# Optimization experiments

Measured on AMD Instinct MI355X. Metric: run time of the kernel, lower is better.

## Reference

```python
import jax, jax.numpy as jnp
import numpy as np

N, D_IN, D_OUT, N_CLASSES = 4096, 1024, 256, 64


def setup_inputs() -> dict:
    key = jax.random.key(0)
    k1, k2, k3, k4 = jax.random.split(key, 4)
    x = jax.random.normal(k1, (N, D_IN), dtype=jnp.float32)
    W = jax.random.normal(k2, (D_IN, D_OUT), dtype=jnp.float32) * 0.02
    b = jax.random.normal(k3, (D_OUT,), dtype=jnp.float32) * 0.02
    targets = jax.random.randint(k4, (N,), 0, N_CLASSES, dtype=jnp.int64)
    return {"x": x, "W": W, "b": b, "targets": targets}


def reference(x, W, b, targets):
    # FC projection (activation = 'linear')
    h = jnp.matmul(x, W) + b                      # [N, d]
    # Pairwise euclidean distances D[i, j] = ||h_i - h_j||_2, matching
    # tf.norm(tf.abs(anchor - others), axis=1) in the original per-anchor loop.
    sq = jnp.sum(h * h, axis=1)                   # [N]
    d2 = sq[:, None] + sq[None, :] - 2.0 * jnp.matmul(h, h.T)
    dist = jnp.sqrt(jnp.maximum(d2, 0.0))         # [N, N]
    same = targets[:, None] == targets[None, :]   # class_division mask
    inf = jnp.float32(np.inf)
    # Hardest positive: max distance among same-class (includes self at 0,
    hardest_pos = jnp.max(jnp.where(same, dist, -inf), axis=1)  # [N]
    # Hardest negative: min distance among different-class samples.
    hardest_neg = jnp.min(jnp.where(same, inf, dist), axis=1)   # [N]
    loss = jnp.sum(jnp.log1p(jnp.exp(hardest_pos - hardest_neg)))
    return loss
```

## Files before the change

kernel.cpp:

```cpp
#include <hip/hip_runtime.h>
#include <math.h>

#define NROWS 4096
#define DIN   1024
#define DOUT  256
#define NPAIR 528

using bfrag = __attribute__((ext_vector_type(8))) short;
using ffrag = __attribute__((ext_vector_type(4))) float;


static __device__ __forceinline__ unsigned short f2bf(float f) {
    unsigned int u = __float_as_uint(f);
    u = (u + 0x7fffu + ((u >> 16) & 1u)) >> 16;
    return (unsigned short)u;
}
static __device__ __forceinline__ unsigned int pack2(float lo, float hi) {
    return (unsigned int)f2bf(lo) | ((unsigned int)f2bf(hi) << 16);
}
static __device__ __forceinline__ unsigned int fkey(float f) {
    unsigned int b = __float_as_uint(f);
    return (b & 0x80000000u) ? ~b : (b | 0x80000000u);
}
static __device__ __forceinline__ float funkey(unsigned int u) {
    return __uint_as_float((u & 0x80000000u) ? (u & 0x7fffffffu) : ~u);
}

__global__ __launch_bounds__(256) void setup(const float* __restrict__ W,
                                             unsigned short* __restrict__ Ws,
                                             float* __restrict__ sq,
                                             unsigned int* __restrict__ pmaxk,
                                             unsigned int* __restrict__ pmink,
                                             float* __restrict__ out) {
    const int f = blockIdx.x * 256 + threadIdx.x;
    {
        const int l  = f & 63;
        const int ks = (f >> 6) & 31;
        const int nt = f >> 11;
        const int col = nt * 16 + (l & 15);
        const int k0  = ks * 32 + (l >> 4) * 8;
        float a[8];
#pragma unroll
        for (int j = 0; j < 8; ++j) a[j] = W[(size_t)(k0 + j) * DOUT + col];
        uint4 v;
        v.x = pack2(a[0], a[1]);
        v.y = pack2(a[2], a[3]);
        v.z = pack2(a[4], a[5]);
        v.w = pack2(a[6], a[7]);
        *(uint4*)&Ws[(size_t)f * 8] = v;
    }
    if (f < NROWS) {
        sq[f]    = 0.0f;
        pmaxk[f] = 0u;
        pmink[f] = 0xFFFFFFFFu;
    }
    if (f == 0) *out = 0.0f;
}

__global__ __launch_bounds__(1024) void gemm1_direct(
    const float* __restrict__ x, const unsigned short* __restrict__ Ws,
    const float* __restrict__ b,
    unsigned short* __restrict__ hs, float* __restrict__ sq) {
    __shared__ __align__(16) short Axs[32 * 528];
    __shared__ __align__(16) short T[16][16][36];

    const int tid = threadIdx.x;
    const int w   = tid >> 6;
    const int l   = tid & 63;
    const int m16 = l & 15;
    const int q   = l >> 4;
    const int t   = blockIdx.x;

    const float* xrow = x + (size_t)(t * 16 + w) * DIN;
#pragma unroll
    for (int s = 0; s < 2; ++s) {
        const int c = s * 512 + l * 8;
        const float4 p0 = *(const float4*)(xrow + c);
        const float4 p1 = *(const float4*)(xrow + c + 4);
        uint4 v;
        v.x = pack2(p0.x, p0.y);
        v.y = pack2(p0.z, p0.w);
        v.z = pack2(p1.x, p1.y);
        v.w = pack2(p1.z, p1.w);
        const int ks = c >> 5;
        const int lw = ((c >> 3) & 3) * 16 + w;
        *(uint4*)&Axs[ks * 528 + lw * 8] = v;
    }
    __syncthreads();

    const bfrag* B = (const bfrag*)Ws + ((size_t)w * 32) * 64 + l;
    ffrag acc = {};
#pragma unroll
    for (int ks = 0; ks < 32; ++ks) {
        const bfrag a = *(const bfrag*)&Axs[ks * 528 + l * 8];
        acc = __builtin_amdgcn_mfma_f32_16x16x32_bf16(a, B[ks * 64], acc, 0, 0, 0);
    }

    const float bc = b[w * 16 + m16];
    float hv[4];
#pragma unroll
    for (int reg = 0; reg < 4; ++reg) hv[reg] = acc[reg] + bc;

#pragma unroll
    for (int reg = 0; reg < 4; ++reg) {
        float p = hv[reg] * hv[reg];
#pragma unroll
        for (int mask = 1; mask < 16; mask <<= 1) p += __shfl_xor(p, mask);
        if (m16 == 0) atomicAdd(&sq[t * 16 + q * 4 + reg], p);
    }

#pragma unroll
    for (int reg = 0; reg < 4; ++reg)
        T[w][q * 4 + reg][m16] = f2bf(hv[reg]);
    __syncthreads();

    if (tid < 512) {
        const int ks = tid >> 6;
        const int ll = tid & 63;
        const int qq = ll >> 4;
        bfrag v = *(const bfrag*)&T[2 * ks + (qq >> 1)][ll & 15][(qq & 1) * 8];
        ((bfrag*)hs)[((size_t)t * 8 + ks) * 64 + ll] = v;
    }
}

__global__ __launch_bounds__(256) void hardest_tri(
    const unsigned short* __restrict__ hs, const float* __restrict__ sq,
    const int* __restrict__ targets,
    unsigned int* __restrict__ pmaxk, unsigned int* __restrict__ pmink) {
    const int tid = threadIdx.x;
    const int w   = tid >> 6;
    const int wi  = w & 1, wj = w >> 1;
    const int l   = tid & 63;
    const int m16 = l & 15;
    const int q   = l >> 4;

    const int k = blockIdx.x;
    int bj = (int)((sqrtf(8.0f * (float)k + 1.0f) - 1.0f) * 0.5f);
    while ((bj + 1) * (bj + 2) / 2 <= k) ++bj;
    while (bj * (bj + 1) / 2 > k) --bj;
    const int bi = k - bj * (bj + 1) / 2;
    const bool diag = (bi == bj);

    const int iw = bi * 128 + wi * 64;
    const int jw = bj * 128 + wj * 64;
    const int tA = iw >> 4;
    const int tB = jw >> 4;

    ffrag acc[4][4] = {};

#pragma unroll
    for (int ks = 0; ks < 8; ++ks) {
        bfrag a[4], bb[4];
#pragma unroll
        for (int mi = 0; mi < 4; ++mi)
            a[mi] = *(const bfrag*)&hs[(((size_t)(tA + mi) * 8 + ks) * 64 + l) * 8];
#pragma unroll
        for (int nj = 0; nj < 4; ++nj)
            bb[nj] = *(const bfrag*)&hs[(((size_t)(tB + nj) * 8 + ks) * 64 + l) * 8];
#pragma unroll
        for (int mi = 0; mi < 4; ++mi)
#pragma unroll
            for (int nj = 0; nj < 4; ++nj)
                acc[mi][nj] = __builtin_amdgcn_mfma_f32_16x16x32_bf16(
                    a[mi], bb[nj], acc[mi][nj], 0, 0, 0);
    }

    int   tj[4];
    float svj[4];
#pragma unroll
    for (int nj = 0; nj < 4; ++nj) {
        const int col = jw + nj * 16 + m16;
        tj[nj]  = targets[col];
        svj[nj] = sq[col];
    }

    float cmx[4], cmn[4];
#pragma unroll
    for (int nj = 0; nj < 4; ++nj) { cmx[nj] = -INFINITY; cmn[nj] = INFINITY; }

#pragma unroll
    for (int mi = 0; mi < 4; ++mi)
#pragma unroll
        for (int reg = 0; reg < 4; ++reg) {
            const int row = iw + mi * 16 + q * 4 + reg;
            const int ti  = targets[row];
            const float si = sq[row];
            float mx = -INFINITY, mn = INFINITY;
#pragma unroll
            for (int nj = 0; nj < 4; ++nj) {
                const float g    = acc[mi][nj][reg];
                const float vrow = fmaf(-2.0f, g, svj[nj]);
                const float vcol = fmaf(-2.0f, g, si);
                if (tj[nj] == ti) {
                    mx = fmaxf(mx, vrow);
                    cmx[nj] = fmaxf(cmx[nj], vcol);
                } else {
                    mn = fminf(mn, vrow);
                    cmn[nj] = fminf(cmn[nj], vcol);
                }
            }
#pragma unroll
            for (int mask = 1; mask < 16; mask <<= 1) {
                mx = fmaxf(mx, __shfl_xor(mx, mask));
                mn = fminf(mn, __shfl_xor(mn, mask));
            }
            if (m16 == 0) {
                atomicMax(&pmaxk[row], fkey(mx));
                atomicMin(&pmink[row], fkey(mn));
            }
        }

    if (!diag) {
#pragma unroll
        for (int nj = 0; nj < 4; ++nj) {
            float mx = cmx[nj], mn = cmn[nj];
            mx = fmaxf(mx, __shfl_xor(mx, 16));
            mn = fminf(mn, __shfl_xor(mn, 16));
            mx = fmaxf(mx, __shfl_xor(mx, 32));
            mn = fminf(mn, __shfl_xor(mn, 32));
            if (q == 0) {
                const int col = jw + nj * 16 + m16;
                atomicMax(&pmaxk[col], fkey(mx));
                atomicMin(&pmink[col], fkey(mn));
            }
        }
    }
}

__global__ __launch_bounds__(256) void finalize(const float* __restrict__ sq,
                                                const unsigned int* __restrict__ pmaxk,
                                                const unsigned int* __restrict__ pmink,
                                                float* __restrict__ out) {
    __shared__ float wsum[4];
    const int i = blockIdx.x * 256 + threadIdx.x;
    const float mp = funkey(pmaxk[i]);
    const float mn = funkey(pmink[i]);
    const float si = sq[i];
    const float hp = sqrtf(fmaxf(si + mp, 0.0f));
    const float hn = sqrtf(fmaxf(si + mn, 0.0f));
    const float d  = hp - hn;
    float li = fmaxf(d, 0.0f) + log1pf(expf(-fabsf(d)));
#pragma unroll
    for (int off = 32; off; off >>= 1) li += __shfl_down(li, off);
    const int lane = threadIdx.x & 63, wv = threadIdx.x >> 6;
    if (lane == 0) wsum[wv] = li;
    __syncthreads();
    if (threadIdx.x == 0)
        atomicAdd(out, wsum[0] + wsum[1] + wsum[2] + wsum[3]);
}

extern "C" void kernel_launch(void* const* d_in, const int* in_sizes, int n_in,
                              void* d_out, int out_size, void* d_ws, size_t ws_size,
                              hipStream_t stream) {
    const float* x       = (const float*)d_in[0];
    const float* W       = (const float*)d_in[1];
    const float* b       = (const float*)d_in[2];
    const int*   targets = (const int*)d_in[3];
    float* out = (float*)d_out;

    unsigned short* Ws    = (unsigned short*)d_ws;
    unsigned short* hs    = Ws + DOUT * DIN;
    float*          sq    = (float*)(hs + NROWS * DOUT);
    unsigned int*   pmaxk = (unsigned int*)(sq + NROWS);
    unsigned int*   pmink = pmaxk + NROWS;

    setup<<<16 * 32 * 64 / 256, 256, 0, stream>>>(W, Ws, sq, pmaxk, pmink, out);
    gemm1_direct<<<NROWS / 16, 1024, 0, stream>>>(x, Ws, b, hs, sq);
    hardest_tri<<<NPAIR, 256, 0, stream>>>(hs, sq, targets, pmaxk, pmink);
    finalize<<<NROWS / 256, 256, 0, stream>>>(sq, pmaxk, pmink, out);
}
```

Measured before the change: 98.36 us.

## Fuse all four stages into one persistent kernel with grid barriers

Replaces the setup, GEMM, pairwise-hardest and finalize launches with a single persistent kernel of 512 blocks that uses atomic-counter grid barriers between phases. The projection GEMM is split into half-width blocks of 256 threads, each computing two output tiles per wave. The aim is to remove inter-kernel launch gaps and tail effects. In exchange it adds global barrier spin costs, relies on all 512 blocks being co-resident, and adds a memset launch to reset the barrier counter.

```diff
diff --git a/kernel.cpp b/kernel.cpp
--- a/kernel.cpp
+++ b/kernel.cpp
@@ -5,6 +5,7 @@
 #define DIN   1024
 #define DOUT  256
 #define NPAIR 528
+#define GRID  512
 
 using bfrag = __attribute__((ext_vector_type(8))) short;
 using ffrag = __attribute__((ext_vector_type(4))) float;
@@ -26,19 +27,40 @@
     return __uint_as_float((u & 0x80000000u) ? (u & 0x7fffffffu) : ~u);
 }
 
-__global__ __launch_bounds__(256) void setup(const float* __restrict__ W,
-                                             unsigned short* __restrict__ Ws,
-                                             float* __restrict__ sq,
-                                             unsigned int* __restrict__ pmaxk,
-                                             unsigned int* __restrict__ pmink,
-                                             float* __restrict__ out) {
-    const int f = blockIdx.x * 256 + threadIdx.x;
-    {
-        const int l  = f & 63;
+static __device__ __forceinline__ void gridbar(unsigned int* bar, unsigned int target) {
+    __syncthreads();
+    if (threadIdx.x == 0) {
+        __hip_atomic_fetch_add(bar, 1u, __ATOMIC_ACQ_REL, __HIP_MEMORY_SCOPE_AGENT);
+        while (__hip_atomic_load(bar, __ATOMIC_ACQUIRE, __HIP_MEMORY_SCOPE_AGENT) < target)
+            __builtin_amdgcn_s_sleep(1);
+    }
+    __syncthreads();
+}
+
+__global__ __launch_bounds__(256, 2) void fused(
+    const float* __restrict__ x, const float* __restrict__ W,
+    const float* __restrict__ bv, const int* __restrict__ targets,
+    unsigned short* __restrict__ Ws, unsigned short* __restrict__ hs,
+    float* __restrict__ sq, unsigned int* __restrict__ pmaxk,
+    unsigned int* __restrict__ pmink, unsigned int* __restrict__ bar,
+    float* __restrict__ out) {
+    __shared__ __align__(16) short Axs[32 * 528];
+    __shared__ __align__(16) short T[8][16][36];
+    __shared__ float wsum[4];
+
+    const int tid = threadIdx.x;
+    const int bid = blockIdx.x;
+    const int w   = tid >> 6;
+    const int l   = tid & 63;
+    const int m16 = l & 15;
+    const int q   = l >> 4;
+
+    if (tid < 64) {
+        const int f  = bid * 64 + tid;
         const int ks = (f >> 6) & 31;
         const int nt = f >> 11;
-        const int col = nt * 16 + (l & 15);
-        const int k0  = ks * 32 + (l >> 4) * 8;
+        const int col = nt * 16 + m16;
+        const int k0  = ks * 32 + q * 8;
         float a[8];
 #pragma unroll
         for (int j = 0; j < 8; ++j) a[j] = W[(size_t)(k0 + j) * DOUT + col];
@@ -48,205 +70,196 @@
         v.z = pack2(a[4], a[5]);
         v.w = pack2(a[6], a[7]);
         *(uint4*)&Ws[(size_t)f * 8] = v;
-    }
-    if (f < NROWS) {
-        sq[f]    = 0.0f;
-        pmaxk[f] = 0u;
-        pmink[f] = 0xFFFFFFFFu;
-    }
-    if (f == 0) *out = 0.0f;
-}
-
-__global__ __launch_bounds__(1024) void gemm1_direct(
-    const float* __restrict__ x, const unsigned short* __restrict__ Ws,
-    const float* __restrict__ b,
-    unsigned short* __restrict__ hs, float* __restrict__ sq) {
-    __shared__ __align__(16) short Axs[32 * 528];
-    __shared__ __align__(16) short T[16][16][36];
-
-    const int tid = threadIdx.x;
-    const int w   = tid >> 6;
-    const int l   = tid & 63;
-    const int m16 = l & 15;
-    const int q   = l >> 4;
-    const int t   = blockIdx.x;
-
-    const float* xrow = x + (size_t)(t * 16 + w) * DIN;
-#pragma unroll
-    for (int s = 0; s < 2; ++s) {
-        const int c = s * 512 + l * 8;
-        const float4 p0 = *(const float4*)(xrow + c);
-        const float4 p1 = *(const float4*)(xrow + c + 4);
-        uint4 v;
-        v.x = pack2(p0.x, p0.y);
-        v.y = pack2(p0.z, p0.w);
-        v.z = pack2(p1.x, p1.y);
-        v.w = pack2(p1.z, p1.w);
-        const int ks = c >> 5;
-        const int lw = ((c >> 3) & 3) * 16 + w;
-        *(uint4*)&Axs[ks * 528 + lw * 8] = v;
-    }
-    __syncthreads();
-
-    const bfrag* B = (const bfrag*)Ws + ((size_t)w * 32) * 64 + l;
-    ffrag acc = {};
-#pragma unroll
-    for (int ks = 0; ks < 32; ++ks) {
-        const bfrag a = *(const bfrag*)&Axs[ks * 528 + l * 8];
-        acc = __builtin_amdgcn_mfma_f32_16x16x32_bf16(a, B[ks * 64], acc, 0, 0, 0);
-    }
-
-    const float bc = b[w * 16 + m16];
-    float hv[4];
-#pragma unroll
-    for (int reg = 0; reg < 4; ++reg) hv[reg] = acc[reg] + bc;
-
-#pragma unroll
-    for (int reg = 0; reg < 4; ++reg) {
-        float p = hv[reg] * hv[reg];
-#pragma unroll
-        for (int mask = 1; mask < 16; mask <<= 1) p += __shfl_xor(p, mask);
-        if (m16 == 0) atomicAdd(&sq[t * 16 + q * 4 + reg], p);
-    }
-
-#pragma unroll
-    for (int reg = 0; reg < 4; ++reg)
-        T[w][q * 4 + reg][m16] = f2bf(hv[reg]);
-    __syncthreads();
-
-    if (tid < 512) {
-        const int ks = tid >> 6;
-        const int ll = tid & 63;
-        const int qq = ll >> 4;
-        bfrag v = *(const bfrag*)&T[2 * ks + (qq >> 1)][ll & 15][(qq & 1) * 8];
-        ((bfrag*)hs)[((size_t)t * 8 + ks) * 64 + ll] = v;
-    }
-}
-
-__global__ __launch_bounds__(256) void hardest_tri(
-    const unsigned short* __restrict__ hs, const float* __restrict__ sq,
-    const int* __restrict__ targets,
-    unsigned int* __restrict__ pmaxk, unsigned int* __restrict__ pmink) {
-    const int tid = threadIdx.x;
-    const int w   = tid >> 6;
-    const int wi  = w & 1, wj = w >> 1;
-    const int l   = tid & 63;
-    const int m16 = l & 15;
-    const int q   = l >> 4;
-
-    const int k = blockIdx.x;
-    int bj = (int)((sqrtf(8.0f * (float)k + 1.0f) - 1.0f) * 0.5f);
-    while ((bj + 1) * (bj + 2) / 2 <= k) ++bj;
-    while (bj * (bj + 1) / 2 > k) --bj;
-    const int bi = k - bj * (bj + 1) / 2;
-    const bool diag = (bi == bj);
-
-    const int iw = bi * 128 + wi * 64;
-    const int jw = bj * 128 + wj * 64;
-    const int tA = iw >> 4;
-    const int tB = jw >> 4;
-
-    ffrag acc[4][4] = {};
-
-#pragma unroll
-    for (int ks = 0; ks < 8; ++ks) {
-        bfrag a[4], bb[4];
+    } else if (tid < 72) {
+        const int i = bid * 8 + (tid - 64);
+        sq[i]    = 0.0f;
+        pmaxk[i] = 0u;
+        pmink[i] = 0xFFFFFFFFu;
+    } else if (tid == 72 && bid == 0) {
+        *out = 0.0f;
+    }
+    gridbar(bar, GRID);
+
+    {
+        const int t    = bid >> 1;
+        const int half = bid & 1;
+
+#pragma unroll
+        for (int rr = 0; rr < 4; ++rr) {
+            const int row = w * 4 + rr;
+            const float* xrow = x + (size_t)(t * 16 + row) * DIN;
+#pragma unroll
+            for (int s = 0; s < 2; ++s) {
+                const int c = s * 512 + l * 8;
+                const float4 p0 = *(const float4*)(xrow + c);
+                const float4 p1 = *(const float4*)(xrow + c + 4);
+                uint4 v;
+                v.x = pack2(p0.x, p0.y);
+                v.y = pack2(p0.z, p0.w);
+                v.z = pack2(p1.x, p1.y);
+                v.w = pack2(p1.z, p1.w);
+                const int ks = c >> 5;
+                const int lw = ((c >> 3) & 3) * 16 + row;
+                *(uint4*)&Axs[ks * 528 + lw * 8] = v;
+            }
+        }
+        __syncthreads();
+
+        const int nt0 = half * 8 + w * 2;
+        const bfrag* B0 = (const bfrag*)Ws + ((size_t)nt0 * 32) * 64 + l;
+        ffrag acc0 = {};
+        ffrag acc1 = {};
+#pragma unroll
+        for (int ks = 0; ks < 32; ++ks) {
+            const bfrag a = *(const bfrag*)&Axs[ks * 528 + l * 8];
+            acc0 = __builtin_amdgcn_mfma_f32_16x16x32_bf16(a, B0[ks * 64], acc0, 0, 0, 0);
+            acc1 = __builtin_amdgcn_mfma_f32_16x16x32_bf16(a, B0[2048 + ks * 64], acc1, 0, 0, 0);
+        }
+
+        float pr[4];
+        {
+            const float bc0 = bv[nt0 * 16 + m16];
+            const float bc1 = bv[(nt0 + 1) * 16 + m16];
+#pragma unroll
+            for (int reg = 0; reg < 4; ++reg) {
+                const float h0 = acc0[reg] + bc0;
+                const float h1 = acc1[reg] + bc1;
+                pr[reg] = h0 * h0 + h1 * h1;
+                T[w * 2][q * 4 + reg][m16]     = f2bf(h0);
+                T[w * 2 + 1][q * 4 + reg][m16] = f2bf(h1);
+            }
+        }
+#pragma unroll
+        for (int reg = 0; reg < 4; ++reg) {
+            float pp = pr[reg];
+#pragma unroll
+            for (int mask = 1; mask < 16; mask <<= 1) pp += __shfl_xor(pp, mask);
+            if (m16 == 0) atomicAdd(&sq[t * 16 + q * 4 + reg], pp);
+        }
+        __syncthreads();
+
+        {
+            const int ksl = tid >> 6;
+            const int ks  = half * 4 + ksl;
+            const int qq  = l >> 4;
+            bfrag v = *(const bfrag*)&T[2 * ksl + (qq >> 1)][l & 15][(qq & 1) * 8];
+            ((bfrag*)hs)[((size_t)t * 8 + ks) * 64 + l] = v;
+        }
+    }
+    gridbar(bar, 2 * GRID);
+
+    for (int k = bid; k < NPAIR; k += GRID) {
+        const int wi = w & 1, wj = w >> 1;
+
+        int bj = (int)((sqrtf(8.0f * (float)k + 1.0f) - 1.0f) * 0.5f);
+        while ((bj + 1) * (bj + 2) / 2 <= k) ++bj;
+        while (bj * (bj + 1) / 2 > k) --bj;
+        const int bi = k - bj * (bj + 1) / 2;
+        const bool diag = (bi == bj);
+
+        const int iw = bi * 128 + wi * 64;
+        const int jw = bj * 128 + wj * 64;
+        const int tA = iw >> 4;
+        const int tB = jw >> 4;
+
+        ffrag acc[4][4] = {};
+
+#pragma unroll
+        for (int ks = 0; ks < 8; ++ks) {
+            bfrag a[4], bb[4];
+#pragma unroll
+            for (int mi = 0; mi < 4; ++mi)
+                a[mi] = *(const bfrag*)&hs[(((size_t)(tA + mi) * 8 + ks) * 64 + l) * 8];
+#pragma unroll
+            for (int nj = 0; nj < 4; ++nj)
+                bb[nj] = *(const bfrag*)&hs[(((size_t)(tB + nj) * 8 + ks) * 64 + l) * 8];
+#pragma unroll
+            for (int mi = 0; mi < 4; ++mi)
+#pragma unroll
+                for (int nj = 0; nj < 4; ++nj)
+                    acc[mi][nj] = __builtin_amdgcn_mfma_f32_16x16x32_bf16(
+                        a[mi], bb[nj], acc[mi][nj], 0, 0, 0);
+        }
+
+        int   tj[4];
+        float svj[4];
+#pragma unroll
+        for (int nj = 0; nj < 4; ++nj) {
+            const int col = jw + nj * 16 + m16;
+            tj[nj]  = targets[col];
+            svj[nj] = sq[col];
+        }
+
+        float cmx[4], cmn[4];
+#pragma unroll
+        for (int nj = 0; nj < 4; ++nj) { cmx[nj] = -INFINITY; cmn[nj] = INFINITY; }
+
 #pragma unroll
         for (int mi = 0; mi < 4; ++mi)
-            a[mi] = *(const bfrag*)&hs[(((size_t)(tA + mi) * 8 + ks) * 64 + l) * 8];
-#pragma unroll
-        for (int nj = 0; nj < 4; ++nj)
-            bb[nj] = *(const bfrag*)&hs[(((size_t)(tB + nj) * 8 + ks) * 64 + l) * 8];
-#pragma unroll
-        for (int mi = 0; mi < 4; ++mi)
-#pragma unroll
-            for (int nj = 0; nj < 4; ++nj)
-                acc[mi][nj] = __builtin_amdgcn_mfma_f32_16x16x32_bf16(
-                    a[mi], bb[nj], acc[mi][nj], 0, 0, 0);
-    }
-
-    int   tj[4];
-    float svj[4];
-#pragma unroll
-    for (int nj = 0; nj < 4; ++nj) {
-        const int col = jw + nj * 16 + m16;
-        tj[nj]  = targets[col];
-        svj[nj] = sq[col];
-    }
-
-    float cmx[4], cmn[4];
-#pragma unroll
-    for (int nj = 0; nj < 4; ++nj) { cmx[nj] = -INFINITY; cmn[nj] = INFINITY; }
-
-#pragma unroll
-    for (int mi = 0; mi < 4; ++mi)
-#pragma unroll
-        for (int reg = 0; reg < 4; ++reg) {
-            const int row = iw + mi * 16 + q * 4 + reg;
-            const int ti  = targets[row];
-            const float si = sq[row];
-            float mx = -INFINITY, mn = INFINITY;
+#pragma unroll
+            for (int reg = 0; reg < 4; ++reg) {
+                const int row = iw + mi * 16 + q * 4 + reg;
+                const int ti  = targets[row];
+                const float si = sq[row];
+                float mx = -INFINITY, mn = INFINITY;
+#pragma unroll
+                for (int nj = 0; nj < 4; ++nj) {
+                    const float g    = acc[mi][nj][reg];
+                    const float vrow = fmaf(-2.0f, g, svj[nj]);
+                    const float vcol = fmaf(-2.0f, g, si);
+                    if (tj[nj] == ti) {
+                        mx = fmaxf(mx, vrow);
+                        cmx[nj] = fmaxf(cmx[nj], vcol);
+                    } else {
+                        mn = fminf(mn, vrow);
+                        cmn[nj] = fminf(cmn[nj], vcol);
+                    }
+                }
+#pragma unroll
+                for (int mask = 1; mask < 16; mask <<= 1) {
+                    mx = fmaxf(mx, __shfl_xor(mx, mask));
+                    mn = fminf(mn, __shfl_xor(mn, mask));
+                }
+                if (m16 == 0) {
+                    atomicMax(&pmaxk[row], fkey(mx));
+                    atomicMin(&pmink[row], fkey(mn));
+                }
+            }
+
+        if (!diag) {
 #pragma unroll
             for (int nj = 0; nj < 4; ++nj) {
-                const float g    = acc[mi][nj][reg];
-                const float vrow = fmaf(-2.0f, g, svj[nj]);
-                const float vcol = fmaf(-2.0f, g, si);
-                if (tj[nj] == ti) {
-                    mx = fmaxf(mx, vrow);
-                    cmx[nj] = fmaxf(cmx[nj], vcol);
-                } else {
-                    mn = fminf(mn, vrow);
-                    cmn[nj] = fminf(cmn[nj], vcol);
-                }
-            }
-#pragma unroll
-            for (int mask = 1; mask < 16; mask <<= 1) {
-                mx = fmaxf(mx, __shfl_xor(mx, mask));
-                mn = fminf(mn, __shfl_xor(mn, mask));
-            }
-            if (m16 == 0) {
-                atomicMax(&pmaxk[row], fkey(mx));
-                atomicMin(&pmink[row], fkey(mn));
-            }
-        }
-
-    if (!diag) {
-#pragma unroll
-        for (int nj = 0; nj < 4; ++nj) {
-            float mx = cmx[nj], mn = cmn[nj];
-            mx = fmaxf(mx, __shfl_xor(mx, 16));
-            mn = fminf(mn, __shfl_xor(mn, 16));
-            mx = fmaxf(mx, __shfl_xor(mx, 32));
-            mn = fminf(mn, __shfl_xor(mn, 32));
-            if (q == 0) {
-                const int col = jw + nj * 16 + m16;
-                atomicMax(&pmaxk[col], fkey(mx));
-                atomicMin(&pmink[col], fkey(mn));
-            }
-        }
-    }
-}
-
-__global__ __launch_bounds__(256) void finalize(const float* __restrict__ sq,
-                                                const unsigned int* __restrict__ pmaxk,
-                                                const unsigned int* __restrict__ pmink,
-                                                float* __restrict__ out) {
-    __shared__ float wsum[4];
-    const int i = blockIdx.x * 256 + threadIdx.x;
-    const float mp = funkey(pmaxk[i]);
-    const float mn = funkey(pmink[i]);
-    const float si = sq[i];
-    const float hp = sqrtf(fmaxf(si + mp, 0.0f));
-    const float hn = sqrtf(fmaxf(si + mn, 0.0f));
-    const float d  = hp - hn;
-    float li = fmaxf(d, 0.0f) + log1pf(expf(-fabsf(d)));
-#pragma unroll
-    for (int off = 32; off; off >>= 1) li += __shfl_down(li, off);
-    const int lane = threadIdx.x & 63, wv = threadIdx.x >> 6;
-    if (lane == 0) wsum[wv] = li;
-    __syncthreads();
-    if (threadIdx.x == 0)
-        atomicAdd(out, wsum[0] + wsum[1] + wsum[2] + wsum[3]);
+                float mx = cmx[nj], mn = cmn[nj];
+                mx = fmaxf(mx, __shfl_xor(mx, 16));
+                mn = fminf(mn, __shfl_xor(mn, 16));
+                mx = fmaxf(mx, __shfl_xor(mx, 32));
+                mn = fminf(mn, __shfl_xor(mn, 32));
+                if (q == 0) {
+                    const int col = jw + nj * 16 + m16;
+                    atomicMax(&pmaxk[col], fkey(mx));
+                    atomicMin(&pmink[col], fkey(mn));
+                }
+            }
+        }
+    }
+    gridbar(bar, 3 * GRID);
+
+    if (bid < NROWS / 256) {
+        const int i = bid * 256 + tid;
+        const float mp = funkey(pmaxk[i]);
+        const float mn = funkey(pmink[i]);
+        const float si = sq[i];
+        const float hp = sqrtf(fmaxf(si + mp, 0.0f));
+        const float hn = sqrtf(fmaxf(si + mn, 0.0f));
+        const float d  = hp - hn;
+        float li = fmaxf(d, 0.0f) + log1pf(expf(-fabsf(d)));
+#pragma unroll
+        for (int off = 32; off; off >>= 1) li += __shfl_down(li, off);
+        if (l == 0) wsum[w] = li;
+        __syncthreads();
+        if (tid == 0)
+            atomicAdd(out, wsum[0] + wsum[1] + wsum[2] + wsum[3]);
+    }
 }
 
 extern "C" void kernel_launch(void* const* d_in, const int* in_sizes, int n_in,
@@ -254,7 +267,7 @@
                               hipStream_t stream) {
     const float* x       = (const float*)d_in[0];
     const float* W       = (const float*)d_in[1];
-    const float* b       = (const float*)d_in[2];
+    const float* bv      = (const float*)d_in[2];
     const int*   targets = (const int*)d_in[3];
     float* out = (float*)d_out;
 
@@ -263,9 +276,9 @@
     float*          sq    = (float*)(hs + NROWS * DOUT);
     unsigned int*   pmaxk = (unsigned int*)(sq + NROWS);
     unsigned int*   pmink = pmaxk + NROWS;
-
-    setup<<<16 * 32 * 64 / 256, 256, 0, stream>>>(W, Ws, sq, pmaxk, pmink, out);
-    gemm1_direct<<<NROWS / 16, 1024, 0, stream>>>(x, Ws, b, hs, sq);
-    hardest_tri<<<NPAIR, 256, 0, stream>>>(hs, sq, targets, pmaxk, pmink);
-    finalize<<<NROWS / 256, 256, 0, stream>>>(sq, pmaxk, pmink, out);
-}
+    unsigned int*   bar   = pmink + NROWS;
+
+    hipMemsetAsync(bar, 0, 16, stream);
+    fused<<<GRID, 256, 0, stream>>>(x, W, bv, targets, Ws, hs, sq,
+                                    pmaxk, pmink, bar, out);
+}
```

New measurement: 253.8 us. 2.58x slower.
